# Kernel optimization log

Hardware: AMD Instinct MI355X
Metric: run time of the kernel (lower is better)

Reference implementation:

```python
import jax, jax.numpy as jnp
import numpy as np

# dummy values used when the merging vehicle does not exist (repo config constants)
DUMMY_EM_DELTA_X = 100.0
DUMMY_EM_DELTA_V = 0.0

B, T, PROJ, MERG, H = 32768, 50, 64, 3, 128
IN_DIM = PROJ + 6 + MERG  # 73


def setup_inputs() -> dict:
    key = jax.random.key(0)
    ks = jax.random.split(key, 8)
    return {
        "proj_belief": jax.random.normal(ks[0], (B, PROJ), dtype=jnp.float32),
        "idm_s": jax.random.uniform(ks[1], (B, T, 12), dtype=jnp.float32),
        "merger_cs": jax.random.normal(ks[2], (B, T, MERG), dtype=jnp.float32),
        "W1": jax.random.normal(ks[3], (IN_DIM, H), dtype=jnp.float32) * (1.0 / np.sqrt(IN_DIM)),
        "b1": jnp.zeros((H,), dtype=jnp.float32),
        "W2": jax.random.normal(ks[4], (H, H), dtype=jnp.float32) * (1.0 / np.sqrt(H)),
        "b2": jnp.zeros((H,), dtype=jnp.float32),
        "W3": jax.random.normal(ks[5], (H, 1), dtype=jnp.float32) * (1.0 / np.sqrt(H)),
        "b3": jnp.zeros((1,), dtype=jnp.float32),
        "scaler_mean": jax.random.uniform(ks[6], (6,), dtype=jnp.float32),
        "scaler_var": jax.random.uniform(ks[7], (6,), dtype=jnp.float32) + 0.5,  # positive variance
        "rollout_len": T,
    }


def reference(proj_belief, idm_s, merger_cs, W1, b1, W2, b2, W3, b3,
              scaler_mean, scaler_var, rollout_len):
    inv_std = 1.0 / jnp.sqrt(scaler_var)

    # time-major slices for scan: [T, B, F]
    idm_t = jnp.swapaxes(idm_s, 0, 1)[:rollout_len]
    merg_t = jnp.swapaxes(merger_cs, 0, 1)[:rollout_len]
    first_t = jnp.arange(rollout_len) == 0

    def step(carry, xs):
        ego_v, ego_x, act = carry  # each [B, 1]
        s, mc, first = xs          # s: [B,12], mc: [B,MERG], first: scalar bool
        f_veh_v = s[:, 1:2]
        m_veh_v = s[:, 2:3]
        f_veh_glob_x = s[:, 4:5]
        m_veh_glob_x = s[:, 5:6]
        m_veh_exists = s[:, 11:12]

        # physics update (dt = 0.1); step 0 initializes from idm_s
        ego_v = jnp.where(first, s[:, 0:1], ego_v + act * 0.1)
        ego_x = jnp.where(first, s[:, 3:4],
                          ego_x + ego_v * 0.1 + 0.5 * act * 0.1 ** 2)

        ef_delta_x = f_veh_glob_x - ego_x
        em_delta_x = (m_veh_glob_x - ego_x) * m_veh_exists \
                     + (1.0 - m_veh_exists) * DUMMY_EM_DELTA_X
        ef_dv = ego_v - f_veh_v
        em_dv = (ego_v - m_veh_v) * m_veh_exists \
                + (1.0 - m_veh_exists) * DUMMY_EM_DELTA_V

        env = jnp.concatenate([ego_v, f_veh_v, ef_dv, ef_delta_x, em_dv, em_delta_x], axis=-1)
        env = (env - scaler_mean) * inv_std

        inp = jnp.concatenate([proj_belief, env, mc], axis=-1)  # [B, 73]
        h = jax.nn.relu(inp @ W1 + b1)
        h = jax.nn.relu(h @ W2 + b2)
        act = h @ W3 + b3  # [B, 1]
        return (ego_v, ego_x, act), act

    zero = jnp.zeros((proj_belief.shape[0], 1), dtype=proj_belief.dtype)
    _, acts = jax.lax.scan(step, (zero, zero, zero), (idm_t, merg_t, first_t))
    return jnp.swapaxes(acts, 0, 1)  # [B, T, 1]
```

## Files before the change

kernel.cpp:

```cpp
#include <hip/hip_runtime.h>
#include <math.h>
#include <stdint.h>

namespace {

constexpr int T = 50;
constexpr int NB = 32768;
constexpr int H = 128;
constexpr int NTHREADS = 256;
constexpr int BLK_ROWS = 32;
constexpr int SH_STRIDE = 132;

typedef float v4f __attribute__((ext_vector_type(4)));
typedef float v2f __attribute__((ext_vector_type(2)));
typedef unsigned int v4u __attribute__((ext_vector_type(4)));
typedef short short8 __attribute__((ext_vector_type(8)));

union FU { float f; uint32_t u; };
union U8 { uint32_t u[4]; short8 v; };

__device__ __forceinline__ uint32_t perm_hi(uint32_t odd, uint32_t even) {
  return __builtin_amdgcn_perm(odd, even, 0x07060302u);
}
__device__ __forceinline__ uint32_t perm_lo(uint32_t odd, uint32_t even) {
  return __builtin_amdgcn_perm(odd, even, 0x05040100u);
}

__device__ __forceinline__ void split2raw(float a, uint32_t& araw, uint32_t& rraw) {
  FU c0; c0.f = a;
  FU fh; fh.u = c0.u & 0xFFFF0000u;
  FU r;  r.f  = a - fh.f;
  araw = c0.u; rraw = r.u;
}
__device__ __forceinline__ void split3(float a, uint32_t& hi, uint32_t& mid, uint32_t& lo) {
  FU c0; c0.f = a;
  uint32_t uh = c0.u & 0xFFFF0000u;
  FU fh; fh.u = uh;
  float r1 = a - fh.f;
  FU c1; c1.f = r1;
  uint32_t um = c1.u & 0xFFFF0000u;
  FU fm; fm.u = um;
  float r2 = r1 - fm.f;
  FU c2; c2.f = r2;
  hi = uh; mid = um; lo = c2.u;
}

__device__ __forceinline__ v4f mfma16(short8 a, short8 b, v4f c) {
  return __builtin_amdgcn_mfma_f32_16x16x32_bf16(a, b, c, 0, 0, 0);
}

__device__ __forceinline__ void block_sync_lds() {
  asm volatile("s_waitcnt lgkmcnt(0)" ::: "memory");
  __builtin_amdgcn_s_barrier();
  asm volatile("" ::: "memory");
}

template<int CTRL>
__device__ __forceinline__ float dpp_radd(float x) {
  FU a; a.f = x;
  FU b; b.u = (uint32_t)__builtin_amdgcn_update_dpp(0, (int)a.u, CTRL, 0xF, 0xF, true);
  return x + b.f;
}
__device__ __forceinline__ float red16(float x) {
  x = dpp_radd<0xB1>(x);
  x = dpp_radd<0x4E>(x);
  x = dpp_radd<0x141>(x);
  x = dpp_radd<0x140>(x);
  return x;
}

__global__ __launch_bounds__(NTHREADS, 2)
void fwdsim9(const float* __restrict__ proj,
             const float* __restrict__ idm,
             const float* __restrict__ merg,
             const float* __restrict__ W1,
             const float* __restrict__ b1,
             const float* __restrict__ W2,
             const float* __restrict__ b2,
             const float* __restrict__ W3,
             const float* __restrict__ b3,
             const float* __restrict__ smean,
             const float* __restrict__ svar,
             float* __restrict__ out)
{
  __shared__ __align__(16) uint32_t sH[BLK_ROWS * SH_STRIDE];
  __shared__ __align__(16) float sAct[2][BLK_ROWS][4];
  __shared__ __align__(16) float sOut[BLK_ROWS * T];

  const int tid  = threadIdx.x;
  const int wave = tid >> 6;
  const int lane = tid & 63;
  const int gq   = lane >> 4;
  const int o    = lane & 15;
  const int row0 = blockIdx.x * BLK_ROWS;

  float istd[6], off[6];
#pragma unroll
  for (int c = 0; c < 6; ++c) {
    istd[c] = 1.0f / sqrtf(svar[c]);
    off[c]  = -smean[c] * istd[c];
  }
  const float b3v = b3[0];
  float b1c[2], b2c[2], W3c[2];
#pragma unroll
  for (int ntl = 0; ntl < 2; ++ntl) {
    const int n = (wave * 2 + ntl) * 16 + o;
    b1c[ntl] = b1[n]; b2c[ntl] = b2[n]; W3c[ntl] = W3[n];
  }

  short8 ebh[2], ebm[2];
#pragma unroll
  for (int ntl = 0; ntl < 2; ++ntl) {
    const int n = (wave * 2 + ntl) * 16 + o;
    uint32_t hr[8], mr[8];
#pragma unroll
    for (int j = 0; j < 8; ++j) {
      const int k = gq * 8 + j;
      const float w = (k < 9) ? W1[(64 + k) * H + n] : 0.f;
      split2raw(w, hr[j], mr[j]);
    }
    U8 fh, fm;
#pragma unroll
    for (int d = 0; d < 4; ++d) {
      fh.u[d] = perm_hi(hr[2*d+1], hr[2*d]);
      fm.u[d] = perm_hi(mr[2*d+1], mr[2*d]);
    }
    ebh[ntl] = fh.v; ebm[ntl] = fm.v;
  }

  short8 w1h[4], w1m[4], w1l[4];
#pragma unroll
  for (int kt = 0; kt < 2; ++kt)
#pragma unroll
    for (int ntl = 0; ntl < 2; ++ntl) {
      const int k0 = kt * 32 + gq * 8;
      const int n  = (wave * 2 + ntl) * 16 + o;
      uint32_t hi[8], mi[8], lo[8];
#pragma unroll
      for (int j = 0; j < 8; ++j) split3(W1[(k0 + j) * H + n], hi[j], mi[j], lo[j]);
      U8 fh, fm, fl;
#pragma unroll
      for (int d = 0; d < 4; ++d) {
        fh.u[d] = perm_hi(hi[2*d+1], hi[2*d]);
        fm.u[d] = perm_hi(mi[2*d+1], mi[2*d]);
        fl.u[d] = perm_hi(lo[2*d+1], lo[2*d]);
      }
      w1h[kt*2+ntl] = fh.v; w1m[kt*2+ntl] = fm.v; w1l[kt*2+ntl] = fl.v;
    }

  v4f base[4];
#pragma unroll
  for (int mt = 0; mt < 2; ++mt) {
    const int row = row0 + mt * 16 + o;
    short8 pah[2], pam[2], pal[2];
#pragma unroll
    for (int kt = 0; kt < 2; ++kt) {
      const float* pp = proj + (size_t)row * 64 + kt * 32 + gq * 8;
      v4f p0 = *(const v4f*)pp;
      v4f p1 = *(const v4f*)(pp + 4);
      uint32_t hi[8], mi[8], lo[8];
#pragma unroll
      for (int e = 0; e < 4; ++e) split3(p0[e], hi[e],   mi[e],   lo[e]);
#pragma unroll
      for (int e = 0; e < 4; ++e) split3(p1[e], hi[4+e], mi[4+e], lo[4+e]);
      U8 uh, um, ul;
#pragma unroll
      for (int d = 0; d < 4; ++d) {
        uh.u[d] = perm_hi(hi[2*d+1], hi[2*d]);
        um.u[d] = perm_hi(mi[2*d+1], mi[2*d]);
        ul.u[d] = perm_hi(lo[2*d+1], lo[2*d]);
      }
      pah[kt] = uh.v; pam[kt] = um.v; pal[kt] = ul.v;
    }
#pragma unroll
    for (int ntl = 0; ntl < 2; ++ntl) {
      v4f acc = (v4f){b1c[ntl], b1c[ntl], b1c[ntl], b1c[ntl]};
#pragma unroll
      for (int kt = 0; kt < 2; ++kt) {
        short8 bh = w1h[kt*2+ntl], bm = w1m[kt*2+ntl], bl = w1l[kt*2+ntl];
        acc = mfma16(pah[kt], bl, acc);
        acc = mfma16(pal[kt], bh, acc);
        acc = mfma16(pam[kt], bm, acc);
        acc = mfma16(pah[kt], bm, acc);
        acc = mfma16(pam[kt], bh, acc);
        acc = mfma16(pah[kt], bh, acc);
      }
      base[mt*2+ntl] = acc;
    }
  }

  short8 w2h[8], w2m[8];
#pragma unroll
  for (int kt = 0; kt < 4; ++kt)
#pragma unroll
    for (int ntl = 0; ntl < 2; ++ntl) {
      const int k0 = kt * 32 + gq * 8;
      const int n  = (wave * 2 + ntl) * 16 + o;
      uint32_t hr[8], mr[8];
#pragma unroll
      for (int j = 0; j < 8; ++j) split2raw(W2[(k0 + j) * H + n], hr[j], mr[j]);
      U8 fh, fm;
#pragma unroll
      for (int d = 0; d < 4; ++d) {
        fh.u[d] = perm_hi(hr[2*d+1], hr[2*d]);
        fm.u[d] = perm_hi(mr[2*d+1], mr[2*d]);
      }
      w2h[kt*2+ntl] = fh.v;
      w2m[kt*2+ntl] = fm.v;
    }

  float ego_v[2], ego_x[2], act[2] = {0.f, 0.f};
  const float* idmp[2];
  const float* mrgp[2];
  v4f sa[2]; v2f fb[2]; float exr[2], m0[2], m1[2], m2[2];
#pragma unroll
  for (int mt = 0; mt < 2; ++mt) {
    idmp[mt] = idm  + (size_t)(row0 + mt*16 + o) * (T*12);
    mrgp[mt] = merg + (size_t)(row0 + mt*16 + o) * (T*3);
    sa[mt] = *(const v4f*)idmp[mt];
    fb[mt] = *(const v2f*)(idmp[mt] + 4);
    exr[mt] = idmp[mt][11];
    m0[mt] = mrgp[mt][0]; m1[mt] = mrgp[mt][1]; m2[mt] = mrgp[mt][2];
  }

  int buf = 0;

#pragma unroll 1
  for (int t = 0; t < T; ++t) {
    float xk[2][9];
#pragma unroll
    for (int mt = 0; mt < 2; ++mt) {
      const float s0 = sa[mt][0], fv = sa[mt][1], mv = sa[mt][2], s3 = sa[mt][3];
      const float fgx = fb[mt][0], mgx = fb[mt][1];
      const float ex = exr[mt];
      if (t == 0) { ego_v[mt] = s0; ego_x[mt] = s3; }
      else {
        ego_v[mt] += act[mt] * 0.1f;
        ego_x[mt] += ego_v[mt] * 0.1f + act[mt] * 0.005f;
      }
      xk[mt][0] = ego_v[mt]                                       * istd[0] + off[0];
      xk[mt][1] = fv                                              * istd[1] + off[1];
      xk[mt][2] = (ego_v[mt] - fv)                                * istd[2] + off[2];
      xk[mt][3] = (fgx - ego_x[mt])                               * istd[3] + off[3];
      xk[mt][4] = ((ego_v[mt] - mv) * ex)                         * istd[4] + off[4];
      xk[mt][5] = ((mgx - ego_x[mt]) * ex + (1.0f - ex) * 100.0f) * istd[5] + off[5];
      xk[mt][6] = m0[mt]; xk[mt][7] = m1[mt]; xk[mt][8] = m2[mt];
    }

    v4f nsa[2]; v2f nfb[2]; float nex[2], nm0[2], nm1[2], nm2[2];
    {
      const int tn = (t + 1 < T) ? t + 1 : t;
#pragma unroll
      for (int mt = 0; mt < 2; ++mt) {
        const float* ip = idmp[mt] + tn * 12;
        nsa[mt] = *(const v4f*)ip;  nfb[mt] = *(const v2f*)(ip + 4);  nex[mt] = ip[11];
        const float* mp = mrgp[mt] + tn * 3;
        nm0[mt] = mp[0]; nm1[mt] = mp[1]; nm2[mt] = mp[2];
      }
    }

#pragma unroll
    for (int mt = 0; mt < 2; ++mt) {
      uint32_t hr[8], mr[8];
#pragma unroll
      for (int j = 0; j < 8; ++j) {
        float v = (gq == 0) ? xk[mt][j] : ((gq == 1 && j == 0) ? xk[mt][8] : 0.f);
        split2raw(v, hr[j], mr[j]);
      }
      U8 uh, um;
#pragma unroll
      for (int d = 0; d < 4; ++d) {
        uh.u[d] = perm_hi(hr[2*d+1], hr[2*d]);
        um.u[d] = perm_hi(mr[2*d+1], mr[2*d]);
      }
      short8 eh = uh.v, em = um.v;

#pragma unroll
      for (int ntl = 0; ntl < 2; ++ntl) {
        v4f a1 = base[mt*2+ntl];
        a1 = mfma16(eh, ebm[ntl], a1);
        a1 = mfma16(em, ebh[ntl], a1);
        a1 = mfma16(eh, ebh[ntl], a1);
#pragma unroll
        for (int r = 0; r < 4; ++r) {
          const float hv = fmaxf(a1[r], 0.f);
          uint32_t hu, ru; split2raw(hv, hu, ru);
          sH[(mt*16 + 4*gq + r) * SH_STRIDE + (wave*2+ntl)*16 + o] = perm_hi(hu, ru);
        }
      }
    }

    block_sync_lds();

#pragma unroll
    for (int mt = 0; mt < 2; ++mt) {
      v4f acc2[2];
#pragma unroll
      for (int ntl = 0; ntl < 2; ++ntl)
        acc2[ntl] = (v4f){b2c[ntl], b2c[ntl], b2c[ntl], b2c[ntl]};

#pragma unroll
      for (int kt = 0; kt < 4; ++kt) {
        const uint32_t* src = &sH[(mt*16 + o) * SH_STRIDE + kt*32 + gq*8];
        v4u q0 = *(const v4u*)src;
        v4u q1 = *(const v4u*)(src + 4);
        U8 uh, um;
        uh.u[0] = perm_hi(q0[1], q0[0]);  um.u[0] = perm_lo(q0[1], q0[0]);
        uh.u[1] = perm_hi(q0[3], q0[2]);  um.u[1] = perm_lo(q0[3], q0[2]);
        uh.u[2] = perm_hi(q1[1], q1[0]);  um.u[2] = perm_lo(q1[1], q1[0]);
        uh.u[3] = perm_hi(q1[3], q1[2]);  um.u[3] = perm_lo(q1[3], q1[2]);
        short8 ah = uh.v, am = um.v;
#pragma unroll
        for (int ntl = 0; ntl < 2; ++ntl) {
          acc2[ntl] = mfma16(ah, w2m[kt*2+ntl], acc2[ntl]);
          acc2[ntl] = mfma16(am, w2h[kt*2+ntl], acc2[ntl]);
          acc2[ntl] = mfma16(ah, w2h[kt*2+ntl], acc2[ntl]);
        }
      }

      v4f part = (v4f){0.f, 0.f, 0.f, 0.f};
#pragma unroll
      for (int ntl = 0; ntl < 2; ++ntl)
#pragma unroll
        for (int r = 0; r < 4; ++r)
          part[r] += fmaxf(acc2[ntl][r], 0.f) * W3c[ntl];
#pragma unroll
      for (int r = 0; r < 4; ++r) part[r] = red16(part[r]);

      const float pv = (o & 2) ? ((o & 1) ? part[3] : part[2])
                               : ((o & 1) ? part[1] : part[0]);
      if (o < 4) sAct[buf][mt*16 + 4*gq + o][wave] = pv;
    }

    block_sync_lds();

#pragma unroll
    for (int mt = 0; mt < 2; ++mt) {
      v4f pa = *(const v4f*)&sAct[buf][mt*16 + o][0];
      act[mt] = ((pa[0] + pa[1]) + (pa[2] + pa[3])) + b3v;
    }
    if (wave == 0 && gq == 0) {
#pragma unroll
      for (int mt = 0; mt < 2; ++mt)
        sOut[(mt*16 + o) * T + t] = act[mt];
    }

#pragma unroll
    for (int mt = 0; mt < 2; ++mt) {
      sa[mt] = nsa[mt]; fb[mt] = nfb[mt]; exr[mt] = nex[mt];
      m0[mt] = nm0[mt]; m1[mt] = nm1[mt]; m2[mt] = nm2[mt];
    }
    buf ^= 1;
  }

  block_sync_lds();
  float* obase = out + (size_t)row0 * T;
  for (int idx = tid; idx < BLK_ROWS * T; idx += NTHREADS)
    obase[idx] = sOut[idx];
}

}

extern "C" void kernel_launch(void* const* d_in, const int* in_sizes, int n_in,
                              void* d_out, int out_size, void* d_ws, size_t ws_size,
                              hipStream_t stream) {
  const float* proj  = (const float*)d_in[0];
  const float* idm   = (const float*)d_in[1];
  const float* merg  = (const float*)d_in[2];
  const float* W1    = (const float*)d_in[3];
  const float* b1    = (const float*)d_in[4];
  const float* W2    = (const float*)d_in[5];
  const float* b2    = (const float*)d_in[6];
  const float* W3    = (const float*)d_in[7];
  const float* b3    = (const float*)d_in[8];
  const float* smean = (const float*)d_in[9];
  const float* svar  = (const float*)d_in[10];

  dim3 grid(NB / BLK_ROWS);
  dim3 block(NTHREADS);
  hipLaunchKernelGGL(fwdsim9, grid, block, 0, stream,
                     proj, idm, merg, W1, b1, W2, b2, W3, b3, smean, svar,
                     (float*)d_out);
}
```

Baseline: 372.8 us.

## Cut register pressure to fit three blocks per CU via LDS base staging

Raises launch bounds from 2 to 3 blocks per SM. To fit, the precomputed layer-1 base (projection part of W1 product) moves from registers into a shared-memory array, and the scaler constants become wave-uniform through readfirstlane so they can live in scalar registers. Pointer arrays become 32-bit byte offsets, and the next-step input loads write straight into the current registers, dropping the double-buffered copies. The cost is an extra LDS read per step and more LDS per block, plus possible spills or less overlap of the next-step prefetch.

Result: no change. 367.2 us (-1.5%).

```diff
diff --git a/kernel.cpp b/kernel.cpp
--- a/kernel.cpp
+++ b/kernel.cpp
@@ -24,6 +24,12 @@
 }
 __device__ __forceinline__ uint32_t perm_lo(uint32_t odd, uint32_t even) {
   return __builtin_amdgcn_perm(odd, even, 0x05040100u);
+}
+
+__device__ __forceinline__ float rfl(float x) {
+  FU a; a.f = x;
+  FU b; b.u = (uint32_t)__builtin_amdgcn_readfirstlane((int)a.u);
+  return b.f;
 }
 
 __device__ __forceinline__ void split2raw(float a, uint32_t& araw, uint32_t& rraw) {
@@ -69,21 +75,22 @@
   return x;
 }
 
-__global__ __launch_bounds__(NTHREADS, 2)
-void fwdsim9(const float* __restrict__ proj,
-             const float* __restrict__ idm,
-             const float* __restrict__ merg,
-             const float* __restrict__ W1,
-             const float* __restrict__ b1,
-             const float* __restrict__ W2,
-             const float* __restrict__ b2,
-             const float* __restrict__ W3,
-             const float* __restrict__ b3,
-             const float* __restrict__ smean,
-             const float* __restrict__ svar,
-             float* __restrict__ out)
+__global__ __launch_bounds__(NTHREADS, 3)
+void fwdsim11(const float* __restrict__ proj,
+              const float* __restrict__ idm,
+              const float* __restrict__ merg,
+              const float* __restrict__ W1,
+              const float* __restrict__ b1,
+              const float* __restrict__ W2,
+              const float* __restrict__ b2,
+              const float* __restrict__ W3,
+              const float* __restrict__ b3,
+              const float* __restrict__ smean,
+              const float* __restrict__ svar,
+              float* __restrict__ out)
 {
   __shared__ __align__(16) uint32_t sH[BLK_ROWS * SH_STRIDE];
+  __shared__ __align__(16) float sBase[128 * 36];
   __shared__ __align__(16) float sAct[2][BLK_ROWS][4];
   __shared__ __align__(16) float sOut[BLK_ROWS * T];
 
@@ -97,15 +104,16 @@
   float istd[6], off[6];
 #pragma unroll
   for (int c = 0; c < 6; ++c) {
-    istd[c] = 1.0f / sqrtf(svar[c]);
-    off[c]  = -smean[c] * istd[c];
-  }
-  const float b3v = b3[0];
-  float b1c[2], b2c[2], W3c[2];
+    const float is = rfl(1.0f / sqrtf(svar[c]));
+    istd[c] = is;
+    off[c]  = rfl(-smean[c] * is);
+  }
+  const float b3v = rfl(b3[0]);
+  float b2c[2], W3c[2];
 #pragma unroll
   for (int ntl = 0; ntl < 2; ++ntl) {
     const int n = (wave * 2 + ntl) * 16 + o;
-    b1c[ntl] = b1[n]; b2c[ntl] = b2[n]; W3c[ntl] = W3[n];
+    b2c[ntl] = b2[n]; W3c[ntl] = W3[n];
   }
 
   short8 ebh[2], ebm[2];
@@ -128,64 +136,69 @@
     ebh[ntl] = fh.v; ebm[ntl] = fm.v;
   }
 
-  short8 w1h[4], w1m[4], w1l[4];
-#pragma unroll
-  for (int kt = 0; kt < 2; ++kt)
-#pragma unroll
-    for (int ntl = 0; ntl < 2; ++ntl) {
-      const int k0 = kt * 32 + gq * 8;
-      const int n  = (wave * 2 + ntl) * 16 + o;
-      uint32_t hi[8], mi[8], lo[8];
-#pragma unroll
-      for (int j = 0; j < 8; ++j) split3(W1[(k0 + j) * H + n], hi[j], mi[j], lo[j]);
-      U8 fh, fm, fl;
-#pragma unroll
-      for (int d = 0; d < 4; ++d) {
-        fh.u[d] = perm_hi(hi[2*d+1], hi[2*d]);
-        fm.u[d] = perm_hi(mi[2*d+1], mi[2*d]);
-        fl.u[d] = perm_hi(lo[2*d+1], lo[2*d]);
-      }
-      w1h[kt*2+ntl] = fh.v; w1m[kt*2+ntl] = fm.v; w1l[kt*2+ntl] = fl.v;
-    }
-
-  v4f base[4];
-#pragma unroll
-  for (int mt = 0; mt < 2; ++mt) {
-    const int row = row0 + mt * 16 + o;
-    short8 pah[2], pam[2], pal[2];
-#pragma unroll
-    for (int kt = 0; kt < 2; ++kt) {
-      const float* pp = proj + (size_t)row * 64 + kt * 32 + gq * 8;
-      v4f p0 = *(const v4f*)pp;
-      v4f p1 = *(const v4f*)(pp + 4);
-      uint32_t hi[8], mi[8], lo[8];
-#pragma unroll
-      for (int e = 0; e < 4; ++e) split3(p0[e], hi[e],   mi[e],   lo[e]);
-#pragma unroll
-      for (int e = 0; e < 4; ++e) split3(p1[e], hi[4+e], mi[4+e], lo[4+e]);
-      U8 uh, um, ul;
-#pragma unroll
-      for (int d = 0; d < 4; ++d) {
-        uh.u[d] = perm_hi(hi[2*d+1], hi[2*d]);
-        um.u[d] = perm_hi(mi[2*d+1], mi[2*d]);
-        ul.u[d] = perm_hi(lo[2*d+1], lo[2*d]);
-      }
-      pah[kt] = uh.v; pam[kt] = um.v; pal[kt] = ul.v;
-    }
-#pragma unroll
-    for (int ntl = 0; ntl < 2; ++ntl) {
-      v4f acc = (v4f){b1c[ntl], b1c[ntl], b1c[ntl], b1c[ntl]};
+  {
+    short8 w1h[4], w1m[4], w1l[4];
+#pragma unroll
+    for (int kt = 0; kt < 2; ++kt)
+#pragma unroll
+      for (int ntl = 0; ntl < 2; ++ntl) {
+        const int k0 = kt * 32 + gq * 8;
+        const int n  = (wave * 2 + ntl) * 16 + o;
+        uint32_t hi[8], mi[8], lo[8];
+#pragma unroll
+        for (int j = 0; j < 8; ++j) split3(W1[(k0 + j) * H + n], hi[j], mi[j], lo[j]);
+        U8 fh, fm, fl;
+#pragma unroll
+        for (int d = 0; d < 4; ++d) {
+          fh.u[d] = perm_hi(hi[2*d+1], hi[2*d]);
+          fm.u[d] = perm_hi(mi[2*d+1], mi[2*d]);
+          fl.u[d] = perm_hi(lo[2*d+1], lo[2*d]);
+        }
+        w1h[kt*2+ntl] = fh.v; w1m[kt*2+ntl] = fm.v; w1l[kt*2+ntl] = fl.v;
+      }
+
+    float b1c[2];
+#pragma unroll
+    for (int ntl = 0; ntl < 2; ++ntl) b1c[ntl] = b1[(wave*2+ntl)*16 + o];
+
+#pragma unroll
+    for (int mt = 0; mt < 2; ++mt) {
+      const int row = row0 + mt * 16 + o;
+      short8 pah[2], pam[2], pal[2];
 #pragma unroll
       for (int kt = 0; kt < 2; ++kt) {
-        short8 bh = w1h[kt*2+ntl], bm = w1m[kt*2+ntl], bl = w1l[kt*2+ntl];
-        acc = mfma16(pah[kt], bl, acc);
-        acc = mfma16(pal[kt], bh, acc);
-        acc = mfma16(pam[kt], bm, acc);
-        acc = mfma16(pah[kt], bm, acc);
-        acc = mfma16(pam[kt], bh, acc);
-        acc = mfma16(pah[kt], bh, acc);
-      }
-      base[mt*2+ntl] = acc;
+        const float* pp = proj + (size_t)row * 64 + kt * 32 + gq * 8;
+        v4f p0 = *(const v4f*)pp;
+        v4f p1 = *(const v4f*)(pp + 4);
+        uint32_t hi[8], mi[8], lo[8];
+#pragma unroll
+        for (int e = 0; e < 4; ++e) split3(p0[e], hi[e],   mi[e],   lo[e]);
+#pragma unroll
+        for (int e = 0; e < 4; ++e) split3(p1[e], hi[4+e], mi[4+e], lo[4+e]);
+        U8 uh, um, ul;
+#pragma unroll
+        for (int d = 0; d < 4; ++d) {
+          uh.u[d] = perm_hi(hi[2*d+1], hi[2*d]);
+          um.u[d] = perm_hi(mi[2*d+1], mi[2*d]);
+          ul.u[d] = perm_hi(lo[2*d+1], lo[2*d]);
+        }
+        pah[kt] = uh.v; pam[kt] = um.v; pal[kt] = ul.v;
+      }
+#pragma unroll
+      for (int ntl = 0; ntl < 2; ++ntl) {
+        v4f acc = (v4f){b1c[ntl], b1c[ntl], b1c[ntl], b1c[ntl]};
+#pragma unroll
+        for (int kt = 0; kt < 2; ++kt) {
+          short8 bh = w1h[kt*2+ntl], bm = w1m[kt*2+ntl], bl = w1l[kt*2+ntl];
+          acc = mfma16(pah[kt], bl, acc);
+          acc = mfma16(pal[kt], bh, acc);
+          acc = mfma16(pam[kt], bm, acc);
+          acc = mfma16(pah[kt], bm, acc);
+          acc = mfma16(pam[kt], bh, acc);
+          acc = mfma16(pah[kt], bh, acc);
+        }
+        *(v4f*)&sBase[(((wave*2+ntl)*16 + o) * 36) + mt*16 + 4*gq] = acc;
+      }
     }
   }
 
@@ -210,19 +223,24 @@
     }
 
   float ego_v[2], ego_x[2], act[2] = {0.f, 0.f};
-  const float* idmp[2];
-  const float* mrgp[2];
+  uint32_t ib[2], mb[2];
   v4f sa[2]; v2f fb[2]; float exr[2], m0[2], m1[2], m2[2];
 #pragma unroll
   for (int mt = 0; mt < 2; ++mt) {
-    idmp[mt] = idm  + (size_t)(row0 + mt*16 + o) * (T*12);
-    mrgp[mt] = merg + (size_t)(row0 + mt*16 + o) * (T*3);
-    sa[mt] = *(const v4f*)idmp[mt];
-    fb[mt] = *(const v2f*)(idmp[mt] + 4);
-    exr[mt] = idmp[mt][11];
-    m0[mt] = mrgp[mt][0]; m1[mt] = mrgp[mt][1]; m2[mt] = mrgp[mt][2];
-  }
-
+    const uint32_t row = row0 + mt*16 + o;
+    ib[mt] = row * (uint32_t)(T*12*4);
+    mb[mt] = row * (uint32_t)(T*3*4);
+    const char* ip = (const char*)idm + ib[mt];
+    sa[mt] = *(const v4f*)ip;
+    fb[mt] = *(const v2f*)(ip + 16);
+    exr[mt] = *(const float*)(ip + 44);
+    const char* mp = (const char*)merg + mb[mt];
+    m0[mt] = *(const float*)mp;
+    m1[mt] = *(const float*)(mp + 4);
+    m2[mt] = *(const float*)(mp + 8);
+  }
+
+  block_sync_lds();
   int buf = 0;
 
 #pragma unroll 1
@@ -247,15 +265,19 @@
       xk[mt][6] = m0[mt]; xk[mt][7] = m1[mt]; xk[mt][8] = m2[mt];
     }
 
-    v4f nsa[2]; v2f nfb[2]; float nex[2], nm0[2], nm1[2], nm2[2];
     {
-      const int tn = (t + 1 < T) ? t + 1 : t;
+      const uint32_t adv = (t + 1 < T) ? 1u : 0u;
 #pragma unroll
       for (int mt = 0; mt < 2; ++mt) {
-        const float* ip = idmp[mt] + tn * 12;
-        nsa[mt] = *(const v4f*)ip;  nfb[mt] = *(const v2f*)(ip + 4);  nex[mt] = ip[11];
-        const float* mp = mrgp[mt] + tn * 3;
-        nm0[mt] = mp[0]; nm1[mt] = mp[1]; nm2[mt] = mp[2];
+        ib[mt] += adv * 48u; mb[mt] += adv * 12u;
+        const char* ip = (const char*)idm + ib[mt];
+        sa[mt] = *(const v4f*)ip;
+        fb[mt] = *(const v2f*)(ip + 16);
+        exr[mt] = *(const float*)(ip + 44);
+        const char* mp = (const char*)merg + mb[mt];
+        m0[mt] = *(const float*)mp;
+        m1[mt] = *(const float*)(mp + 4);
+        m2[mt] = *(const float*)(mp + 8);
       }
     }
 
@@ -277,7 +299,7 @@
 
 #pragma unroll
       for (int ntl = 0; ntl < 2; ++ntl) {
-        v4f a1 = base[mt*2+ntl];
+        v4f a1 = *(const v4f*)&sBase[(((wave*2+ntl)*16 + o) * 36) + mt*16 + 4*gq];
         a1 = mfma16(eh, ebm[ntl], a1);
         a1 = mfma16(em, ebh[ntl], a1);
         a1 = mfma16(eh, ebh[ntl], a1);
@@ -343,12 +365,6 @@
 #pragma unroll
       for (int mt = 0; mt < 2; ++mt)
         sOut[(mt*16 + o) * T + t] = act[mt];
-    }
-
-#pragma unroll
-    for (int mt = 0; mt < 2; ++mt) {
-      sa[mt] = nsa[mt]; fb[mt] = nfb[mt]; exr[mt] = nex[mt];
-      m0[mt] = nm0[mt]; m1[mt] = nm1[mt]; m2[mt] = nm2[mt];
     }
     buf ^= 1;
   }
@@ -378,7 +394,7 @@
 
   dim3 grid(NB / BLK_ROWS);
   dim3 block(NTHREADS);
-  hipLaunchKernelGGL(fwdsim9, grid, block, 0, stream,
+  hipLaunchKernelGGL(fwdsim11, grid, block, 0, stream,
                      proj, idm, merg, W1, b1, W2, b2, W3, b3, smean, svar,
                      (float*)d_out);
 }
```
